# Kernel optimization log

Hardware: AMD Instinct MI355X
Metric: run time of the kernel (lower is better)

The kernel has to match this reference:

```python
import jax, jax.numpy as jnp
import numpy as np

H = W = 56
HID = 384
B = 16

def dct_mat(N):
    # Orthonormal DCT-II matrix: X = D @ x, idct via D.T
    n = jnp.arange(N, dtype=jnp.float32)
    k = jnp.arange(N, dtype=jnp.float32)[:, None]
    D = jnp.cos(jnp.pi * (2.0 * n + 1.0) * k / (2.0 * N)) * jnp.sqrt(2.0 / N)
    D = D.at[0].multiply(1.0 / jnp.sqrt(2.0))
    return D

def setup_inputs() -> dict:
    key = jax.random.key(0)
    ks = jax.random.split(key, 16)
    s = 0.02
    return {
        "x": jax.random.normal(ks[0], (B, HID, H, W), dtype=jnp.float32),
        "freq_embed": jax.random.normal(ks[1], (H, W, HID), dtype=jnp.float32),
        "dw_w": jax.random.normal(ks[2], (HID, 1, 3, 3), dtype=jnp.float32) * s,
        "dw_b": jnp.zeros((HID,), jnp.float32),
        "lin_w": jax.random.normal(ks[3], (2 * HID, HID), dtype=jnp.float32) * s,
        "lin_b": jnp.zeros((2 * HID,), jnp.float32),
        "vel_w": jax.random.normal(ks[4], (HID, HID), dtype=jnp.float32) * s,
        "vel_b": jnp.zeros((HID,), jnp.float32),
        "tok_w": jax.random.normal(ks[5], (HID, HID), dtype=jnp.float32) * s,
        "tok_b": jnp.zeros((HID,), jnp.float32),
        "ln_g": jnp.ones((HID,), jnp.float32),
        "ln_b": jnp.zeros((HID,), jnp.float32),
        "out_w": jax.random.normal(ks[6], (HID, HID), dtype=jnp.float32) * s,
        "out_b": jnp.zeros((HID,), jnp.float32),
        "c": jnp.ones((1,), jnp.float32),
        "alpha": jnp.ones((1,), jnp.float32) * 0.1,
    }

def reference(x, freq_embed, dw_w, dw_b, lin_w, lin_b, vel_w, vel_b,
              tok_w, tok_b, ln_g, ln_b, out_w, out_b, c, alpha):
    Bn, C, Hh, Ww = x.shape
    # depthwise 3x3 conv, padding=1
    x = jax.lax.conv_general_dilated(
        x, dw_w, (1, 1), 'SAME',
        dimension_numbers=('NCHW', 'OIHW', 'NCHW'),
        feature_group_count=C) + dw_b[None, :, None, None]
    xl = jnp.transpose(x, (0, 2, 3, 1))            # [B,H,W,C]
    xz = xl @ lin_w.T + lin_b                      # [B,H,W,2C]
    xg, z = jnp.split(xz, 2, axis=-1)
    DH, DW_ = dct_mat(Hh), dct_mat(Ww)
    x_ch = jnp.transpose(xg, (0, 3, 1, 2))         # [B,C,H,W]
    x_u0 = jnp.einsum('ih,jw,bchw->bcij', DH, DW_, x_ch)
    x_vel = xg @ vel_w.T + vel_b                   # [B,H,W,C]
    x_v0 = jnp.einsum('ih,jw,bchw->bcij', DH, DW_, jnp.transpose(x_vel, (0, 3, 1, 2)))
    # decay map exp(-(n^2+m^2)) on linspace(0,pi)
    wn = jnp.linspace(0.0, jnp.pi, Hh + 1)[:Hh][:, None]
    wm = jnp.linspace(0.0, jnp.pi, Ww + 1)[:Ww][None, :]
    decay = jnp.exp(-(wn ** 2 + wm ** 2))[None, None]
    x_u0 = x_u0 * decay
    x_v0 = x_v0 * decay
    # wave modulation from freq embedding (shared across batch)
    t = jax.nn.relu(freq_embed @ tok_w.T + tok_b)  # [H,W,C]
    t = jnp.transpose(t, (2, 0, 1))[None]          # [1,C,H,W]
    eps = 1e-6
    cos_t = jnp.cos(c[0] * t)
    sin_t = jnp.sin(c[0] * t) / (c[0] + eps)
    final = cos_t * x_u0 + sin_t * (x_v0 + 0.5 * alpha[0] * x_u0)
    x_final = jnp.einsum('hi,wj,bchw->bcij', DH, DW_, final)  # IDCT2D
    y = jnp.transpose(x_final, (0, 2, 3, 1))       # [B,H,W,C]
    mu = jnp.mean(y, axis=-1, keepdims=True)
    var = jnp.mean((y - mu) ** 2, axis=-1, keepdims=True)
    yn = (y - mu) / jnp.sqrt(var + 1e-5) * ln_g + ln_b
    gated = yn * jax.nn.silu(z)                    # [B,H,W,C]
    out = gated @ out_w.T + out_b
    return jnp.transpose(out, (0, 3, 1, 2))        # [B,C,H,W]
```

## Files before the change

kernel.cpp:

```cpp
#include <hip/hip_runtime.h>
#include <math.h>

#define HH 56
#define WS_W 56
#define HWS 3136
#define CD 384
#define BB 16
#define NROW (BB*HWS)
#define SLOT ((size_t)NROW*CD)

typedef __attribute__((ext_vector_type(8))) short bf16x8;
typedef __attribute__((ext_vector_type(4))) float f32x4;

__device__ inline ushort f2bf(float v) {
  uint u = __float_as_uint(v);
  uint r = (u + 0x7fffu + ((u >> 16) & 1u)) >> 16;
  return (ushort)r;
}
__device__ inline float bf2f(ushort h) { return __uint_as_float((uint)h << 16); }

__global__ void prep_d_k(float* __restrict__ D) {
  for (int idx = threadIdx.x; idx < HH*HH; idx += blockDim.x) {
    int k = idx / HH, n = idx % HH;
    double v = cos(3.14159265358979323846 * (2.0*n + 1.0) * k / (2.0*HH)) * sqrt(2.0/HH);
    if (k == 0) v *= 0.70710678118654752440;
    D[idx] = (float)v;
  }
}

__global__ __launch_bounds__(256) void split_w_k(
    const float* __restrict__ W, ushort* __restrict__ hi,
    ushort* __restrict__ lo, int nelem) {
  int i = blockIdx.x*256 + threadIdx.x;
  if (i >= nelem) return;
  float v = W[i];
  ushort h = f2bf(v);
  hi[i] = h;
  lo[i] = f2bf(v - bf2f(h));
}

__global__ __launch_bounds__(256) void conv_k(
    const float* __restrict__ x, const float* __restrict__ dww,
    const float* __restrict__ dwb, ushort* __restrict__ xc)
{
  __shared__ float xs[3][58][33];
  __shared__ float wgt[32][9];
  __shared__ float wb[32];
  int t = threadIdx.x;
  int c0 = blockIdx.x * 32, h = blockIdx.y, b = blockIdx.z;
  for (int idx = t; idx < 1344; idx += 256) {
    int wq = idx % 14, rem = idx / 14;
    int dy = rem % 3, ch = rem / 3;
    int gh = h + dy - 1;
    float4 v = {0.f, 0.f, 0.f, 0.f};
    if (gh >= 0 && gh < HH)
      v = *(const float4*)(x + (((size_t)b*CD + c0 + ch)*HH + gh)*WS_W + wq*4);
    int wp = wq*4 + 1;
    xs[dy][wp+0][ch] = v.x;
    xs[dy][wp+1][ch] = v.y;
    xs[dy][wp+2][ch] = v.z;
    xs[dy][wp+3][ch] = v.w;
  }
  if (t < 192) {
    int e = t & 1, dy = (t >> 1) % 3, ch = t / 6;
    xs[dy][e*57][ch] = 0.f;
  }
  for (int idx = t; idx < 288; idx += 256)
    wgt[idx/9][idx%9] = dww[(size_t)(c0 + idx/9)*9 + idx%9];
  if (t < 32) wb[t] = dwb[c0 + t];
  __syncthreads();
  int ch = t & 31, wq8 = t >> 5;
  #pragma unroll
  for (int wwi = 0; wwi < 7; ++wwi) {
    int w = wwi*8 + wq8;
    float acc = wb[ch];
    #pragma unroll
    for (int dy = 0; dy < 3; ++dy)
      #pragma unroll
      for (int dx = 0; dx < 3; ++dx)
        acc = fmaf(wgt[ch][dy*3+dx], xs[dy][w+dx][ch], acc);
    size_t oi = ((size_t)b*HWS + h*WS_W + w)*CD + c0 + ch;
    ushort hh = f2bf(acc);
    xc[oi] = hh;
    xc[SLOT + oi] = f2bf(acc - bf2f(hh));
  }
}

template<int EPI>
__global__ __launch_bounds__(256) void gemm_k(
    const float* __restrict__ A, const float* __restrict__ Bw,
    const float* __restrict__ bias, float* __restrict__ out0,
    float* __restrict__ out1, const float* __restrict__ cptr)
{
  __shared__ float As[16][68];
  __shared__ float Bs[16][68];
  int t = threadIdx.x;
  int col0 = blockIdx.x * 64;
  int row0 = blockIdx.y * 64;
  int lr = t >> 2, lk = (t & 3) * 4;
  const float* Ap = A + (size_t)(row0 + lr)*CD + lk;
  const float* Bp = Bw + (size_t)(col0 + lr)*CD + lk;
  float acc[4][4] = {};
  int tx = t & 15, ty = t >> 4;
  for (int k0 = 0; k0 < CD; k0 += 16) {
    float4 av = *(const float4*)(Ap + k0);
    float4 bv = *(const float4*)(Bp + k0);
    __syncthreads();
    As[lk+0][lr] = av.x; As[lk+1][lr] = av.y; As[lk+2][lr] = av.z; As[lk+3][lr] = av.w;
    Bs[lk+0][lr] = bv.x; Bs[lk+1][lr] = bv.y; Bs[lk+2][lr] = bv.z; Bs[lk+3][lr] = bv.w;
    __syncthreads();
    #pragma unroll
    for (int k = 0; k < 16; ++k) {
      float4 a4 = *(const float4*)&As[k][ty*4];
      float4 b4 = *(const float4*)&Bs[k][tx*4];
      float aa[4] = {a4.x, a4.y, a4.z, a4.w};
      float bbv[4] = {b4.x, b4.y, b4.z, b4.w};
      #pragma unroll
      for (int i = 0; i < 4; ++i)
        #pragma unroll
        for (int j = 0; j < 4; ++j)
          acc[i][j] = fmaf(aa[i], bbv[j], acc[i][j]);
    }
  }
  float cs = 0.f;
  if constexpr (EPI == 2) cs = cptr[0];
  #pragma unroll
  for (int i = 0; i < 4; ++i) {
    int r = row0 + ty*4 + i;
    #pragma unroll
    for (int j = 0; j < 4; ++j) {
      int cg = col0 + tx*4 + j;
      float v = acc[i][j];
      if constexpr (EPI == 2) {
        v += bias[cg];
        v = fmaxf(v, 0.f);
        int pi = r / 56, pj = r % 56;
        float wn = 3.14159265358979323846f/56.f * (float)pi;
        float wm = 3.14159265358979323846f/56.f * (float)pj;
        float dec = expf(-(wn*wn + wm*wm));
        out0[(size_t)r*CD + cg] = cosf(cs*v)*dec;
        out1[(size_t)r*CD + cg] = sinf(cs*v)/(cs + 1e-6f)*dec;
      }
    }
  }
}

template<int EPI>
__global__ __launch_bounds__(256, 2) void mgemm_k(
    const ushort* __restrict__ Ah_g, const ushort* __restrict__ Al_g,
    const ushort* __restrict__ Wh, const ushort* __restrict__ Wl,
    const float* __restrict__ bias,
    float* __restrict__ out0, float* __restrict__ out1,
    const ushort* __restrict__ UinH, const float* __restrict__ cosD,
    const float* __restrict__ sinD, const float* __restrict__ velb,
    const float* __restrict__ alphap)
{
  __shared__ char smem[32768];
  int t = threadIdx.x;
  int nwg = gridDim.x * gridDim.y;
  int wgid = blockIdx.y * gridDim.x + blockIdx.x;
  int cpx = nwg >> 3;
  int sw = (wgid & 7) * cpx + (wgid >> 3);
  int col0 = (sw % gridDim.x) * 128;
  int row0 = (sw / gridDim.x) * 128;

  int r = t >> 1, half = t & 1;
  int n = r & 15, rt = r >> 4, q0 = half * 2;
  const ushort* Ahp = Ah_g + (size_t)(row0 + r)*CD + half*16;
  const ushort* Alp = Al_g + (size_t)(row0 + r)*CD + half*16;
  const ushort* Bhp = Wh + (size_t)(col0 + r)*CD + half*16;
  const ushort* Blp = Wl + (size_t)(col0 + r)*CD + half*16;
  int aoff0 = rt*1024 + (q0*16 + n)*16;
  int aoff1 = rt*1024 + ((q0+1)*16 + n)*16;
  int boff0 = 16384 + aoff0, boff1 = 16384 + aoff1;
  int wid = t >> 6, lane = t & 63;
  int wr = wid >> 1, wc = wid & 1;
  f32x4 acc[4][4];
  #pragma unroll
  for (int i = 0; i < 4; ++i)
    #pragma unroll
    for (int j = 0; j < 4; ++j)
      acc[i][j] = (f32x4){0.f, 0.f, 0.f, 0.f};

  for (int k0 = 0; k0 < CD; k0 += 32) {
    uint4 fh0 = *(const uint4*)(Ahp + k0);
    uint4 fh1 = *(const uint4*)(Ahp + k0 + 8);
    uint4 fl0 = *(const uint4*)(Alp + k0);
    uint4 fl1 = *(const uint4*)(Alp + k0 + 8);
    uint4 bh0 = *(const uint4*)(Bhp + k0);
    uint4 bh1 = *(const uint4*)(Bhp + k0 + 8);
    uint4 bl0 = *(const uint4*)(Blp + k0);
    uint4 bl1 = *(const uint4*)(Blp + k0 + 8);
    __syncthreads();
    *(uint4*)(smem + aoff0)        = fh0;
    *(uint4*)(smem + aoff0 + 8192) = fl0;
    *(uint4*)(smem + aoff1)        = fh1;
    *(uint4*)(smem + aoff1 + 8192) = fl1;
    *(uint4*)(smem + boff0)        = bh0;
    *(uint4*)(smem + boff0 + 8192) = bl0;
    *(uint4*)(smem + boff1)        = bh1;
    *(uint4*)(smem + boff1 + 8192) = bl1;
    __syncthreads();
    bf16x8 Ah[4], Al[4], Bh[4], Bl[4];
    #pragma unroll
    for (int i = 0; i < 4; ++i) {
      int ao = (wr*4 + i)*1024 + lane*16;
      Ah[i] = *(const bf16x8*)(smem + ao);
      Al[i] = *(const bf16x8*)(smem + ao + 8192);
      int bo = 16384 + (wc*4 + i)*1024 + lane*16;
      Bh[i] = *(const bf16x8*)(smem + bo);
      Bl[i] = *(const bf16x8*)(smem + bo + 8192);
    }
    #pragma unroll
    for (int i = 0; i < 4; ++i)
      #pragma unroll
      for (int j = 0; j < 4; ++j) {
        acc[i][j] = __builtin_amdgcn_mfma_f32_16x16x32_bf16(Ah[i], Bh[j], acc[i][j], 0, 0, 0);
        acc[i][j] = __builtin_amdgcn_mfma_f32_16x16x32_bf16(Ah[i], Bl[j], acc[i][j], 0, 0, 0);
        acc[i][j] = __builtin_amdgcn_mfma_f32_16x16x32_bf16(Al[i], Bh[j], acc[i][j], 0, 0, 0);
      }
  }

  int nn = lane & 15, qq = lane >> 4;
  float ahalf = 0.f;
  if constexpr (EPI == 1) ahalf = 0.5f * alphap[0];
  #pragma unroll
  for (int i = 0; i < 4; ++i) {
    #pragma unroll
    for (int j = 0; j < 4; ++j) {
      #pragma unroll
      for (int reg = 0; reg < 4; ++reg) {
        int rg = row0 + wr*64 + i*16 + qq*4 + reg;
        int cg = col0 + wc*64 + j*16 + nn;
        float v = acc[i][j][reg];
        if constexpr (EPI == 0) {
          v += bias[cg];
          if (cg < CD) out0[(size_t)rg*CD + cg] = v;
          else         out1[(size_t)rg*CD + cg - CD] = v;
        } else if constexpr (EPI == 1) {
          int p = rg % HWS;
          size_t uidx = (size_t)rg*CD + cg;
          float u  = bf2f(UinH[uidx]) + bf2f(UinH[SLOT + uidx]);
          float cd = cosD[(size_t)p*CD + cg];
          float sd = sinD[(size_t)p*CD + cg];
          if (p == 0) v += 56.f * velb[cg];
          out0[uidx] = cd*u + sd*(v + ahalf*u);
        } else {
          v += bias[cg];
          int bidx = rg / HWS, hw = rg % HWS;
          out0[((size_t)bidx*CD + cg)*HWS + hw] = v;
        }
      }
    }
  }
}

__global__ __launch_bounds__(448) void dct_k(
    const float* __restrict__ in, float* __restrict__ out,
    const float* __restrict__ D, int NC, int trans, int osplit)
{
  __shared__ float Ds[56][60];
  __shared__ float Xs[56][128];
  int t = threadIdx.x;
  int c0 = blockIdx.x * 128;
  size_t bt = blockIdx.y;
  for (int idx = t; idx < 3136; idx += 448) {
    int k = idx / 56, m = idx % 56;
    Ds[k][m] = trans ? D[k*56 + m] : D[m*56 + k];
  }
  const float* inb = in + bt*56*(size_t)NC + c0;
  for (int fi = t; fi < 56*32; fi += 448) {
    int rw = fi >> 5, cg = fi & 31;
    *(float4*)&Xs[rw][cg*4] = *(const float4*)(inb + (size_t)rw*NC + cg*4);
  }
  __syncthreads();
  int tx = t % 32, ty = t / 32;
  float acc[4][4] = {};
  #pragma unroll 4
  for (int k = 0; k < 56; ++k) {
    float4 a4 = *(const float4*)&Ds[k][ty*4];
    float4 b4 = *(const float4*)&Xs[k][tx*4];
    float aa[4] = {a4.x, a4.y, a4.z, a4.w};
    float bbv[4] = {b4.x, b4.y, b4.z, b4.w};
    #pragma unroll
    for (int i = 0; i < 4; ++i)
      #pragma unroll
      for (int j = 0; j < 4; ++j)
        acc[i][j] = fmaf(aa[i], bbv[j], acc[i][j]);
  }
  if (!osplit) {
    float* ob = out + bt*56*(size_t)NC + c0;
    #pragma unroll
    for (int i = 0; i < 4; ++i) {
      int m = ty*4 + i;
      float4 o; o.x = acc[i][0]; o.y = acc[i][1]; o.z = acc[i][2]; o.w = acc[i][3];
      *(float4*)(ob + (size_t)m*NC + tx*4) = o;
    }
  } else {
    ushort* obh = (ushort*)out;
    size_t base = bt*56*(size_t)NC + c0;
    #pragma unroll
    for (int i = 0; i < 4; ++i) {
      int m = ty*4 + i;
      size_t e = base + (size_t)m*NC + tx*4;
      ushort hs[4], ls[4];
      #pragma unroll
      for (int j = 0; j < 4; ++j) {
        float v = acc[i][j];
        hs[j] = f2bf(v);
        ls[j] = f2bf(v - bf2f(hs[j]));
      }
      uint2 hv, lv;
      hv.x = hs[0] | ((uint)hs[1] << 16); hv.y = hs[2] | ((uint)hs[3] << 16);
      lv.x = ls[0] | ((uint)ls[1] << 16); lv.y = ls[2] | ((uint)ls[3] << 16);
      *(uint2*)(obh + e) = hv;
      *(uint2*)(obh + SLOT + e) = lv;
    }
  }
}

__global__ __launch_bounds__(256) void ln_gate_k(
    const float* __restrict__ Y, const float* __restrict__ Z,
    const float* __restrict__ g, const float* __restrict__ be,
    ushort* __restrict__ out)
{
  int lane = threadIdx.x & 63, wv = threadIdx.x >> 6;
  size_t r = (size_t)blockIdx.x*4 + wv;
  const float* y = Y + r*CD;
  float v[6];
  float s = 0.f;
  #pragma unroll
  for (int q = 0; q < 6; ++q) { v[q] = y[lane + 64*q]; s += v[q]; }
  #pragma unroll
  for (int off = 32; off > 0; off >>= 1) s += __shfl_xor(s, off, 64);
  float mu = s * (1.f/384.f);
  float s2 = 0.f;
  #pragma unroll
  for (int q = 0; q < 6; ++q) { float d = v[q]-mu; s2 += d*d; }
  #pragma unroll
  for (int off = 32; off > 0; off >>= 1) s2 += __shfl_xor(s2, off, 64);
  float rs = 1.f / sqrtf(s2*(1.f/384.f) + 1e-5f);
  #pragma unroll
  for (int q = 0; q < 6; ++q) {
    int c = lane + 64*q;
    float yn = (v[q]-mu)*rs*g[c] + be[c];
    float zv = Z[r*CD + c];
    float sz = zv / (1.f + expf(-zv));
    float gv = yn*sz;
    ushort hh = f2bf(gv);
    out[r*CD + c] = hh;
    out[SLOT + r*CD + c] = f2bf(gv - bf2f(hh));
  }
}

extern "C" void kernel_launch(void* const* d_in, const int* in_sizes, int n_in,
                              void* d_out, int out_size, void* d_ws, size_t ws_size,
                              hipStream_t stream) {
  const float* x     = (const float*)d_in[0];
  const float* fe    = (const float*)d_in[1];
  const float* dw_w  = (const float*)d_in[2];
  const float* dw_b  = (const float*)d_in[3];
  const float* lin_w = (const float*)d_in[4];
  const float* lin_b = (const float*)d_in[5];
  const float* vel_w = (const float*)d_in[6];
  const float* vel_b = (const float*)d_in[7];
  const float* tok_w = (const float*)d_in[8];
  const float* tok_b = (const float*)d_in[9];
  const float* ln_g  = (const float*)d_in[10];
  const float* ln_b  = (const float*)d_in[11];
  const float* out_w = (const float*)d_in[12];
  const float* out_b = (const float*)d_in[13];
  const float* cp    = (const float*)d_in[14];
  const float* ap    = (const float*)d_in[15];

  float* ws    = (float*)d_ws;
  float* slotA = ws;
  float* slotB = ws + SLOT;
  float* slotC = ws + 2*SLOT;
  float* Dm    = ws + 3*SLOT;
  float* cosD  = Dm + 3136;
  float* sinD  = cosD + (size_t)HWS*CD;
  ushort* whi  = (ushort*)(sinD + (size_t)HWS*CD);
  ushort* wlo  = whi + 589824;

  ushort* xcH = (ushort*)slotA;
  ushort* UH  = (ushort*)slotB;
  ushort* GH  = (ushort*)slotB;

  prep_d_k<<<1, 256, 0, stream>>>(Dm);
  split_w_k<<<1152, 256, 0, stream>>>(lin_w, whi,          wlo,          294912);
  split_w_k<<< 576, 256, 0, stream>>>(vel_w, whi + 294912, wlo + 294912, 147456);
  split_w_k<<< 576, 256, 0, stream>>>(out_w, whi + 442368, wlo + 442368, 147456);

  conv_k<<<dim3(12, 56, 16), 256, 0, stream>>>(x, dw_w, dw_b, xcH);
  gemm_k<2><<<dim3(6, 49), 256, 0, stream>>>(fe, tok_w, tok_b, cosD, sinD, cp);
  mgemm_k<0><<<dim3(6, 392), 256, 0, stream>>>(xcH, xcH + SLOT, whi, wlo, lin_b,
      slotB, slotC, nullptr, nullptr, nullptr, nullptr, nullptr);
  dct_k<<<dim3(168, 16), 448, 0, stream>>>(slotB, slotA, Dm, 21504, 0, 0);
  dct_k<<<dim3(3, 896), 448, 0, stream>>>(slotA, slotB, Dm, 384, 0, 1);
  mgemm_k<1><<<dim3(3, 392), 256, 0, stream>>>(UH, UH + SLOT, whi + 294912, wlo + 294912,
      nullptr, slotA, nullptr, UH, cosD, sinD, vel_b, ap);
  dct_k<<<dim3(168, 16), 448, 0, stream>>>(slotA, slotB, Dm, 21504, 1, 0);
  dct_k<<<dim3(3, 896), 448, 0, stream>>>(slotB, slotA, Dm, 384, 1, 0);
  ln_gate_k<<<12544, 256, 0, stream>>>(slotA, slotC, ln_g, ln_b, GH);
  mgemm_k<3><<<dim3(3, 392), 256, 0, stream>>>(GH, GH + SLOT, whi + 442368, wlo + 442368,
      out_b, (float*)d_out, nullptr, nullptr, nullptr, nullptr, nullptr, nullptr);
}
```

Baseline: 744.5 us.

## Fuse separable DCT passes into single 2D DCT kernel with blocked channel layout

Replaces the two separable 1D DCT launches (forward and inverse) with one dct2d kernel per direction. Each block loads a full 56x56 plane for four channels into shared memory and applies both passes there, which removes the intermediate global round trip. The forward output is written in a channel-blocked (groups of 8) bf16 hi/lo layout, so the velocity GEMM gains a new A-operand addressing mode and an updated epilogue index. The cost is heavy shared-memory use with only 56 of 64 lanes active, and strided A loads in the GEMM.

```diff
diff --git a/kernel.cpp b/kernel.cpp
--- a/kernel.cpp
+++ b/kernel.cpp
@@ -145,7 +145,7 @@
   }
 }
 
-template<int EPI>
+template<int EPI, int ALAY>
 __global__ __launch_bounds__(256, 2) void mgemm_k(
     const ushort* __restrict__ Ah_g, const ushort* __restrict__ Al_g,
     const ushort* __restrict__ Wh, const ushort* __restrict__ Wl,
@@ -166,8 +166,16 @@
 
   int r = t >> 1, half = t & 1;
   int n = r & 15, rt = r >> 4, q0 = half * 2;
-  const ushort* Ahp = Ah_g + (size_t)(row0 + r)*CD + half*16;
-  const ushort* Alp = Al_g + (size_t)(row0 + r)*CD + half*16;
+  const ushort* Ahp; const ushort* Alp;
+  if constexpr (ALAY == 0) {
+    Ahp = Ah_g + (size_t)(row0 + r)*CD + half*16;
+    Alp = Al_g + (size_t)(row0 + r)*CD + half*16;
+  } else {
+    int rg = row0 + r; int bb = rg / HWS, p = rg % HWS;
+    size_t base = ((size_t)(bb*48 + half*2)*HWS + p)*8;
+    Ahp = Ah_g + base;
+    Alp = Al_g + base;
+  }
   const ushort* Bhp = Wh + (size_t)(col0 + r)*CD + half*16;
   const ushort* Blp = Wl + (size_t)(col0 + r)*CD + half*16;
   int aoff0 = rt*1024 + (q0*16 + n)*16;
@@ -183,10 +191,19 @@
       acc[i][j] = (f32x4){0.f, 0.f, 0.f, 0.f};
 
   for (int k0 = 0; k0 < CD; k0 += 32) {
-    uint4 fh0 = *(const uint4*)(Ahp + k0);
-    uint4 fh1 = *(const uint4*)(Ahp + k0 + 8);
-    uint4 fl0 = *(const uint4*)(Alp + k0);
-    uint4 fl1 = *(const uint4*)(Alp + k0 + 8);
+    uint4 fh0, fh1, fl0, fl1;
+    if constexpr (ALAY == 0) {
+      fh0 = *(const uint4*)(Ahp + k0);
+      fh1 = *(const uint4*)(Ahp + k0 + 8);
+      fl0 = *(const uint4*)(Alp + k0);
+      fl1 = *(const uint4*)(Alp + k0 + 8);
+    } else {
+      size_t o = (size_t)k0 * HWS;
+      fh0 = *(const uint4*)(Ahp + o);
+      fh1 = *(const uint4*)(Ahp + o + HWS*8);
+      fl0 = *(const uint4*)(Alp + o);
+      fl1 = *(const uint4*)(Alp + o + HWS*8);
+    }
     uint4 bh0 = *(const uint4*)(Bhp + k0);
     uint4 bh1 = *(const uint4*)(Bhp + k0 + 8);
     uint4 bl0 = *(const uint4*)(Blp + k0);
@@ -238,8 +255,8 @@
           if (cg < CD) out0[(size_t)rg*CD + cg] = v;
           else         out1[(size_t)rg*CD + cg - CD] = v;
         } else if constexpr (EPI == 1) {
-          int p = rg % HWS;
-          size_t uidx = (size_t)rg*CD + cg;
+          int p = rg % HWS, bidx = rg / HWS;
+          size_t uidx = ((size_t)(bidx*48 + (cg >> 3))*HWS + p)*8 + (cg & 7);
           float u  = bf2f(UinH[uidx]) + bf2f(UinH[SLOT + uidx]);
           float cd = cosD[(size_t)p*CD + cg];
           float sd = sinD[(size_t)p*CD + cg];
@@ -255,66 +272,136 @@
   }
 }
 
-__global__ __launch_bounds__(448) void dct_k(
+template<int INV>
+__global__ __launch_bounds__(256, 2) void dct2d_k(
     const float* __restrict__ in, float* __restrict__ out,
-    const float* __restrict__ D, int NC, int trans, int osplit)
+    const float* __restrict__ Dm)
 {
-  __shared__ float Ds[56][60];
-  __shared__ float Xs[56][128];
+  __shared__ float Xs[4*3364];
+  __shared__ float M1[3360];
+  __shared__ float M2[3360];
   int t = threadIdx.x;
-  int c0 = blockIdx.x * 128;
-  size_t bt = blockIdx.y;
-  for (int idx = t; idx < 3136; idx += 448) {
-    int k = idx / 56, m = idx % 56;
-    Ds[k][m] = trans ? D[k*56 + m] : D[m*56 + k];
-  }
-  const float* inb = in + bt*56*(size_t)NC + c0;
-  for (int fi = t; fi < 56*32; fi += 448) {
-    int rw = fi >> 5, cg = fi & 31;
-    *(float4*)&Xs[rw][cg*4] = *(const float4*)(inb + (size_t)rw*NC + cg*4);
+  int xb = blockIdx.x;
+  int cg4 = (xb & 7)*12 + (xb >> 3);
+  int b = blockIdx.y;
+  int cb8 = cg4 >> 1, sub4 = (cg4 & 1)*4, c0 = cg4*4;
+
+  for (int idx = t; idx < 3136; idx += 256) {
+    int r_ = idx/56, q_ = idx%56;
+    float dv = Dm[r_*56 + q_];
+    if (INV) { M1[r_*60 + q_] = dv; M2[q_*60 + r_] = dv; }
+    else     { M1[q_*60 + r_] = dv; M2[r_*60 + q_] = dv; }
+  }
+  if (INV) {
+    const float* Fb = in + ((size_t)(b*48 + cb8)*HWS)*8 + sub4;
+    for (int p = t; p < HWS; p += 256) {
+      float4 v = *(const float4*)(Fb + (size_t)p*8);
+      int h = p/56, w = p%56;
+      Xs[0*3364 + h*60 + w] = v.x;
+      Xs[1*3364 + h*60 + w] = v.y;
+      Xs[2*3364 + h*60 + w] = v.z;
+      Xs[3*3364 + h*60 + w] = v.w;
+    }
+  } else {
+    const float* inb = in + (size_t)b*HWS*CD + c0;
+    for (int p = t; p < HWS; p += 256) {
+      float4 v = *(const float4*)(inb + (size_t)p*CD);
+      int h = p/56, w = p%56;
+      Xs[0*3364 + h*60 + w] = v.x;
+      Xs[1*3364 + h*60 + w] = v.y;
+      Xs[2*3364 + h*60 + w] = v.z;
+      Xs[3*3364 + h*60 + w] = v.w;
+    }
   }
   __syncthreads();
-  int tx = t % 32, ty = t / 32;
-  float acc[4][4] = {};
-  #pragma unroll 4
-  for (int k = 0; k < 56; ++k) {
-    float4 a4 = *(const float4*)&Ds[k][ty*4];
-    float4 b4 = *(const float4*)&Xs[k][tx*4];
-    float aa[4] = {a4.x, a4.y, a4.z, a4.w};
-    float bbv[4] = {b4.x, b4.y, b4.z, b4.w};
-    #pragma unroll
-    for (int i = 0; i < 4; ++i)
-      #pragma unroll
-      for (int j = 0; j < 4; ++j)
-        acc[i][j] = fmaf(aa[i], bbv[j], acc[i][j]);
-  }
-  if (!osplit) {
-    float* ob = out + bt*56*(size_t)NC + c0;
-    #pragma unroll
-    for (int i = 0; i < 4; ++i) {
-      int m = ty*4 + i;
-      float4 o; o.x = acc[i][0]; o.y = acc[i][1]; o.z = acc[i][2]; o.w = acc[i][3];
-      *(float4*)(ob + (size_t)m*NC + tx*4) = o;
+
+  int ch = t >> 6, l = t & 63;
+  int jg = l % 14, hg = l / 14;
+  float a2[14][4];
+  if (l < 56) {
+    float* Xc = &Xs[ch*3364];
+    float acc[14][4] = {};
+    for (int w = 0; w < 56; ++w) {
+      float4 m = *(const float4*)&M1[w*60 + jg*4];
+      #pragma unroll
+      for (int ri = 0; ri < 14; ++ri) {
+        float xv = Xc[(hg*14 + ri)*60 + w];
+        acc[ri][0] = fmaf(xv, m.x, acc[ri][0]);
+        acc[ri][1] = fmaf(xv, m.y, acc[ri][1]);
+        acc[ri][2] = fmaf(xv, m.z, acc[ri][2]);
+        acc[ri][3] = fmaf(xv, m.w, acc[ri][3]);
+      }
+    }
+    #pragma unroll
+    for (int ri = 0; ri < 14; ++ri) {
+      float4 o = {acc[ri][0], acc[ri][1], acc[ri][2], acc[ri][3]};
+      *(float4*)&Xc[(hg*14 + ri)*60 + jg*4] = o;
+    }
+    #pragma unroll
+    for (int ri = 0; ri < 14; ++ri) { a2[ri][0]=0.f; a2[ri][1]=0.f; a2[ri][2]=0.f; a2[ri][3]=0.f; }
+    for (int h = 0; h < 56; ++h) {
+      float4 tv = *(const float4*)&Xc[h*60 + jg*4];
+      #pragma unroll
+      for (int ri = 0; ri < 14; ++ri) {
+        float dv = M2[(hg*14 + ri)*60 + h];
+        a2[ri][0] = fmaf(dv, tv.x, a2[ri][0]);
+        a2[ri][1] = fmaf(dv, tv.y, a2[ri][1]);
+        a2[ri][2] = fmaf(dv, tv.z, a2[ri][2]);
+        a2[ri][3] = fmaf(dv, tv.w, a2[ri][3]);
+      }
+    }
+  }
+  __syncthreads();
+  if (l < 56) {
+    if (INV) {
+      float* Yl = Xs;
+      #pragma unroll
+      for (int ri = 0; ri < 14; ++ri) {
+        int p = (hg*14 + ri)*56 + jg*4;
+        float4 o = {a2[ri][0], a2[ri][1], a2[ri][2], a2[ri][3]};
+        *(float4*)&Yl[ch*3140 + p] = o;
+      }
+    } else {
+      ushort* Ul = (ushort*)Xs;
+      #pragma unroll
+      for (int ri = 0; ri < 14; ++ri) {
+        int p = (hg*14 + ri)*56 + jg*4;
+        ushort hs[4], ls[4];
+        #pragma unroll
+        for (int dj = 0; dj < 4; ++dj) {
+          float v = a2[ri][dj];
+          hs[dj] = f2bf(v);
+          ls[dj] = f2bf(v - bf2f(hs[dj]));
+        }
+        uint2 hv, lv;
+        hv.x = hs[0] | ((uint)hs[1] << 16); hv.y = hs[2] | ((uint)hs[3] << 16);
+        lv.x = ls[0] | ((uint)ls[1] << 16); lv.y = ls[2] | ((uint)ls[3] << 16);
+        *(uint2*)&Ul[ch*3136 + p] = hv;
+        *(uint2*)&Ul[12544 + ch*3136 + p] = lv;
+      }
+    }
+  }
+  __syncthreads();
+  if (INV) {
+    const float* Yl = Xs;
+    float* ob = out + (size_t)b*HWS*CD + c0;
+    for (int p = t; p < HWS; p += 256) {
+      float4 o = {Yl[0*3140 + p], Yl[1*3140 + p], Yl[2*3140 + p], Yl[3*3140 + p]};
+      *(float4*)(ob + (size_t)p*CD) = o;
     }
   } else {
-    ushort* obh = (ushort*)out;
-    size_t base = bt*56*(size_t)NC + c0;
-    #pragma unroll
-    for (int i = 0; i < 4; ++i) {
-      int m = ty*4 + i;
-      size_t e = base + (size_t)m*NC + tx*4;
-      ushort hs[4], ls[4];
-      #pragma unroll
-      for (int j = 0; j < 4; ++j) {
-        float v = acc[i][j];
-        hs[j] = f2bf(v);
-        ls[j] = f2bf(v - bf2f(hs[j]));
-      }
-      uint2 hv, lv;
-      hv.x = hs[0] | ((uint)hs[1] << 16); hv.y = hs[2] | ((uint)hs[3] << 16);
-      lv.x = ls[0] | ((uint)ls[1] << 16); lv.y = ls[2] | ((uint)ls[3] << 16);
-      *(uint2*)(obh + e) = hv;
-      *(uint2*)(obh + SLOT + e) = lv;
+    const ushort* Ul = (const ushort*)Xs;
+    ushort* og = (ushort*)out;
+    size_t base = ((size_t)(b*48 + cb8)*HWS)*8 + sub4;
+    for (int idx = t; idx < 2*HWS; idx += 256) {
+      int pl = idx >= HWS;
+      int p = pl ? idx - HWS : idx;
+      ushort u0 = Ul[pl*12544 + 0*3136 + p];
+      ushort u1 = Ul[pl*12544 + 1*3136 + p];
+      ushort u2 = Ul[pl*12544 + 2*3136 + p];
+      ushort u3 = Ul[pl*12544 + 3*3136 + p];
+      uint2 v; v.x = u0 | ((uint)u1 << 16); v.y = u2 | ((uint)u3 << 16);
+      *(uint2*)(og + (size_t)pl*SLOT + base + (size_t)p*8) = v;
     }
   }
 }
@@ -384,7 +471,7 @@
   ushort* wlo  = whi + 589824;
 
   ushort* xcH = (ushort*)slotA;
-  ushort* UH  = (ushort*)slotB;
+  ushort* UH  = (ushort*)slotA;
   ushort* GH  = (ushort*)slotB;
 
   prep_d_k<<<1, 256, 0, stream>>>(Dm);
@@ -394,15 +481,13 @@
 
   conv_k<<<dim3(12, 56, 16), 256, 0, stream>>>(x, dw_w, dw_b, xcH);
   gemm_k<2><<<dim3(6, 49), 256, 0, stream>>>(fe, tok_w, tok_b, cosD, sinD, cp);
-  mgemm_k<0><<<dim3(6, 392), 256, 0, stream>>>(xcH, xcH + SLOT, whi, wlo, lin_b,
+  mgemm_k<0,0><<<dim3(6, 392), 256, 0, stream>>>(xcH, xcH + SLOT, whi, wlo, lin_b,
       slotB, slotC, nullptr, nullptr, nullptr, nullptr, nullptr);
-  dct_k<<<dim3(168, 16), 448, 0, stream>>>(slotB, slotA, Dm, 21504, 0, 0);
-  dct_k<<<dim3(3, 896), 448, 0, stream>>>(slotA, slotB, Dm, 384, 0, 1);
-  mgemm_k<1><<<dim3(3, 392), 256, 0, stream>>>(UH, UH + SLOT, whi + 294912, wlo + 294912,
-      nullptr, slotA, nullptr, UH, cosD, sinD, vel_b, ap);
-  dct_k<<<dim3(168, 16), 448, 0, stream>>>(slotA, slotB, Dm, 21504, 1, 0);
-  dct_k<<<dim3(3, 896), 448, 0, stream>>>(slotB, slotA, Dm, 384, 1, 0);
+  dct2d_k<0><<<dim3(96, 16), 256, 0, stream>>>(slotB, slotA, Dm);
+  mgemm_k<1,1><<<dim3(3, 392), 256, 0, stream>>>(UH, UH + SLOT, whi + 294912, wlo + 294912,
+      nullptr, slotB, nullptr, UH, cosD, sinD, vel_b, ap);
+  dct2d_k<1><<<dim3(96, 16), 256, 0, stream>>>(slotB, slotA, Dm);
   ln_gate_k<<<12544, 256, 0, stream>>>(slotA, slotC, ln_g, ln_b, GH);
-  mgemm_k<3><<<dim3(3, 392), 256, 0, stream>>>(GH, GH + SLOT, whi + 442368, wlo + 442368,
+  mgemm_k<3,0><<<dim3(3, 392), 256, 0, stream>>>(GH, GH + SLOT, whi + 442368, wlo + 442368,
       out_b, (float*)d_out, nullptr, nullptr, nullptr, nullptr, nullptr, nullptr);
 }
```

Measured after the change: 749.9 us. Within noise of the previous version (+0.7%).

## Run DCT transforms on bf16 MFMA with hi/lo split-precision

Applied to the files above, without the earlier changes.

Replaces the four scalar-FMA DCT matrix-multiply kernels with an MFMA-based kernel. Each fp32 operand is split into bf16 hi and lo parts and the product is summed over four MFMA passes to keep near-fp32 accuracy. The DCT matrix is pre-packed into a padded 64x64 swizzled layout and loaded into LDS with global_load_lds. Blocks are remapped with a swizzle for cache locality. This shifts the DCT work off the vector ALUs onto matrix cores, at the cost of extra conversion work, padding waste from 56 to 64, and uncoalesced scalar output stores.

```diff
diff --git a/kernel.cpp b/kernel.cpp
--- a/kernel.cpp
+++ b/kernel.cpp
@@ -19,12 +19,34 @@
 }
 __device__ inline float bf2f(ushort h) { return __uint_as_float((uint)h << 16); }
 
+__device__ inline void gl16(const void* g, void* l) {
+  __builtin_amdgcn_global_load_lds(
+      (const __attribute__((address_space(1))) void*)g,
+      (__attribute__((address_space(3))) void*)l,
+      16, 0, 0);
+}
+
 __global__ void prep_d_k(float* __restrict__ D) {
   for (int idx = threadIdx.x; idx < HH*HH; idx += blockDim.x) {
     int k = idx / HH, n = idx % HH;
     double v = cos(3.14159265358979323846 * (2.0*n + 1.0) * k / (2.0*HH)) * sqrt(2.0/HH);
     if (k == 0) v *= 0.70710678118654752440;
     D[idx] = (float)v;
+  }
+}
+
+__global__ void prep_pack_k(const float* __restrict__ Dm, ushort* __restrict__ Dpk) {
+  for (int idx = threadIdx.x; idx < 2*4096; idx += 256) {
+    int o = idx >> 12, e = idx & 4095;
+    int mg = e >> 10, rem = e & 1023;
+    int j = rem & 7, km = rem >> 3;
+    int koct = km >> 4, m16 = km & 15;
+    int m = mg*16 + m16, k = koct*8 + j;
+    float v = 0.f;
+    if (m < 56 && k < 56) v = o ? Dm[k*56 + m] : Dm[m*56 + k];
+    ushort h = f2bf(v);
+    Dpk[o*8192 + e] = h;
+    Dpk[o*8192 + 4096 + e] = f2bf(v - bf2f(h));
   }
 }
 
@@ -255,66 +277,105 @@
   }
 }
 
-__global__ __launch_bounds__(448) void dct_k(
-    const float* __restrict__ in, float* __restrict__ out,
-    const float* __restrict__ D, int NC, int trans, int osplit)
+template<int OSPLIT>
+__global__ __launch_bounds__(256, 3) void dmm_k(
+    const float* __restrict__ in, float* __restrict__ outf,
+    const ushort* __restrict__ Dpk, int NBT, int RS, size_t BSTR)
 {
-  __shared__ float Ds[56][60];
-  __shared__ float Xs[56][128];
+  __shared__ char smem[49152];
   int t = threadIdx.x;
-  int c0 = blockIdx.x * 128;
-  size_t bt = blockIdx.y;
-  for (int idx = t; idx < 3136; idx += 448) {
-    int k = idx / 56, m = idx % 56;
-    Ds[k][m] = trans ? D[k*56 + m] : D[m*56 + k];
-  }
-  const float* inb = in + bt*56*(size_t)NC + c0;
-  for (int fi = t; fi < 56*32; fi += 448) {
-    int rw = fi >> 5, cg = fi & 31;
-    *(float4*)&Xs[rw][cg*4] = *(const float4*)(inb + (size_t)rw*NC + cg*4);
-  }
-  __syncthreads();
-  int tx = t % 32, ty = t / 32;
-  float acc[4][4] = {};
-  #pragma unroll 4
-  for (int k = 0; k < 56; ++k) {
-    float4 a4 = *(const float4*)&Ds[k][ty*4];
-    float4 b4 = *(const float4*)&Xs[k][tx*4];
-    float aa[4] = {a4.x, a4.y, a4.z, a4.w};
-    float bbv[4] = {b4.x, b4.y, b4.z, b4.w};
+  int flat = blockIdx.x;
+  int sw = (flat & 7) * 336 + (flat >> 3);
+  int batch = sw / NBT, nt0 = sw - batch*NBT;
+  int n0 = nt0 * 128;
+  const float* inb = in + (size_t)batch*BSTR;
+  int wid = t >> 6, lane = t & 63;
+
+  {
+    const char* src = (const char*)Dpk;
     #pragma unroll
     for (int i = 0; i < 4; ++i)
-      #pragma unroll
-      for (int j = 0; j < 4; ++j)
-        acc[i][j] = fmaf(aa[i], bbv[j], acc[i][j]);
-  }
-  if (!osplit) {
-    float* ob = out + bt*56*(size_t)NC + c0;
-    #pragma unroll
-    for (int i = 0; i < 4; ++i) {
-      int m = ty*4 + i;
-      float4 o; o.x = acc[i][0]; o.y = acc[i][1]; o.z = acc[i][2]; o.w = acc[i][3];
-      *(float4*)(ob + (size_t)m*NC + tx*4) = o;
-    }
-  } else {
-    ushort* obh = (ushort*)out;
-    size_t base = bt*56*(size_t)NC + c0;
-    #pragma unroll
-    for (int i = 0; i < 4; ++i) {
-      int m = ty*4 + i;
-      size_t e = base + (size_t)m*NC + tx*4;
-      ushort hs[4], ls[4];
-      #pragma unroll
-      for (int j = 0; j < 4; ++j) {
-        float v = acc[i][j];
+      gl16(src + wid*4096 + i*1024 + lane*16,
+           smem + 32768 + wid*4096 + i*1024);
+  }
+
+  {
+    int koct = t >> 5, c4 = (t & 31) * 4;
+    float4 fr[8];
+    if (koct < 7) {
+      #pragma unroll
+      for (int j = 0; j < 8; ++j)
+        fr[j] = *(const float4*)(inb + (size_t)(koct*8 + j)*RS + n0 + c4);
+    } else {
+      #pragma unroll
+      for (int j = 0; j < 8; ++j) fr[j] = (float4){0.f,0.f,0.f,0.f};
+    }
+    #pragma unroll
+    for (int c = 0; c < 4; ++c) {
+      ushort hs[8], ls[8];
+      #pragma unroll
+      for (int j = 0; j < 8; ++j) {
+        float v = ((const float*)&fr[j])[c];
         hs[j] = f2bf(v);
         ls[j] = f2bf(v - bf2f(hs[j]));
       }
-      uint2 hv, lv;
-      hv.x = hs[0] | ((uint)hs[1] << 16); hv.y = hs[2] | ((uint)hs[3] << 16);
-      lv.x = ls[0] | ((uint)ls[1] << 16); lv.y = ls[2] | ((uint)ls[3] << 16);
-      *(uint2*)(obh + e) = hv;
-      *(uint2*)(obh + SLOT + e) = lv;
+      uint4 hv, lv;
+      hv.x = hs[0]|((uint)hs[1]<<16); hv.y = hs[2]|((uint)hs[3]<<16);
+      hv.z = hs[4]|((uint)hs[5]<<16); hv.w = hs[6]|((uint)hs[7]<<16);
+      lv.x = ls[0]|((uint)ls[1]<<16); lv.y = ls[2]|((uint)ls[3]<<16);
+      lv.z = ls[4]|((uint)ls[5]<<16); lv.w = ls[6]|((uint)ls[7]<<16);
+      int nn = c4 + c;
+      int off = (nn >> 4)*2048 + (koct*16 + ((nn & 15) ^ koct))*16;
+      *(uint4*)(smem + off)         = hv;
+      *(uint4*)(smem + 16384 + off) = lv;
+    }
+  }
+  __syncthreads();
+
+  int mg = wid;
+  bf16x8 Ah[2], Al[2];
+  #pragma unroll
+  for (int ks = 0; ks < 2; ++ks) {
+    int ao = 32768 + mg*2048 + ((ks*4 + (lane>>4))*16 + (lane&15))*16;
+    Ah[ks] = *(const bf16x8*)(smem + ao);
+    Al[ks] = *(const bf16x8*)(smem + ao + 8192);
+  }
+  f32x4 acc[8];
+  #pragma unroll
+  for (int nt = 0; nt < 8; ++nt) acc[nt] = (f32x4){0.f,0.f,0.f,0.f};
+  #pragma unroll
+  for (int nt = 0; nt < 8; ++nt) {
+    #pragma unroll
+    for (int ks = 0; ks < 2; ++ks) {
+      int koctr = ks*4 + (lane>>4);
+      int bo = nt*2048 + (koctr*16 + ((lane & 15) ^ koctr))*16;
+      bf16x8 Bh = *(const bf16x8*)(smem + bo);
+      bf16x8 Bl = *(const bf16x8*)(smem + bo + 16384);
+      acc[nt] = __builtin_amdgcn_mfma_f32_16x16x32_bf16(Ah[ks], Bh, acc[nt], 0, 0, 0);
+      acc[nt] = __builtin_amdgcn_mfma_f32_16x16x32_bf16(Ah[ks], Bl, acc[nt], 0, 0, 0);
+      acc[nt] = __builtin_amdgcn_mfma_f32_16x16x32_bf16(Al[ks], Bh, acc[nt], 0, 0, 0);
+      acc[nt] = __builtin_amdgcn_mfma_f32_16x16x32_bf16(Al[ks], Bl, acc[nt], 0, 0, 0);
+    }
+  }
+
+  int q = lane >> 4, n16 = lane & 15;
+  #pragma unroll
+  for (int nt = 0; nt < 8; ++nt) {
+    #pragma unroll
+    for (int reg = 0; reg < 4; ++reg) {
+      int m = mg*16 + q*4 + reg;
+      if (m < 56) {
+        size_t addr = (size_t)batch*BSTR + (size_t)m*RS + n0 + nt*16 + n16;
+        float v = acc[nt][reg];
+        if constexpr (OSPLIT == 0) {
+          outf[addr] = v;
+        } else {
+          ushort* oh = (ushort*)outf;
+          ushort hh = f2bf(v);
+          oh[addr] = hh;
+          oh[SLOT + addr] = f2bf(v - bf2f(hh));
+        }
+      }
     }
   }
 }
@@ -382,12 +443,14 @@
   float* sinD  = cosD + (size_t)HWS*CD;
   ushort* whi  = (ushort*)(sinD + (size_t)HWS*CD);
   ushort* wlo  = whi + 589824;
+  ushort* Dpk  = wlo + 589824;
 
   ushort* xcH = (ushort*)slotA;
   ushort* UH  = (ushort*)slotB;
   ushort* GH  = (ushort*)slotB;
 
   prep_d_k<<<1, 256, 0, stream>>>(Dm);
+  prep_pack_k<<<1, 256, 0, stream>>>(Dm, Dpk);
   split_w_k<<<1152, 256, 0, stream>>>(lin_w, whi,          wlo,          294912);
   split_w_k<<< 576, 256, 0, stream>>>(vel_w, whi + 294912, wlo + 294912, 147456);
   split_w_k<<< 576, 256, 0, stream>>>(out_w, whi + 442368, wlo + 442368, 147456);
@@ -396,12 +459,12 @@
   gemm_k<2><<<dim3(6, 49), 256, 0, stream>>>(fe, tok_w, tok_b, cosD, sinD, cp);
   mgemm_k<0><<<dim3(6, 392), 256, 0, stream>>>(xcH, xcH + SLOT, whi, wlo, lin_b,
       slotB, slotC, nullptr, nullptr, nullptr, nullptr, nullptr);
-  dct_k<<<dim3(168, 16), 448, 0, stream>>>(slotB, slotA, Dm, 21504, 0, 0);
-  dct_k<<<dim3(3, 896), 448, 0, stream>>>(slotA, slotB, Dm, 384, 0, 1);
+  dmm_k<0><<<2688, 256, 0, stream>>>(slotB, slotA, Dpk,        168, 21504, (size_t)1204224);
+  dmm_k<1><<<2688, 256, 0, stream>>>(slotA, slotB, Dpk,          3,   384, (size_t)21504);
   mgemm_k<1><<<dim3(3, 392), 256, 0, stream>>>(UH, UH + SLOT, whi + 294912, wlo + 294912,
       nullptr, slotA, nullptr, UH, cosD, sinD, vel_b, ap);
-  dct_k<<<dim3(168, 16), 448, 0, stream>>>(slotA, slotB, Dm, 21504, 1, 0);
-  dct_k<<<dim3(3, 896), 448, 0, stream>>>(slotB, slotA, Dm, 384, 1, 0);
+  dmm_k<0><<<2688, 256, 0, stream>>>(slotA, slotB, Dpk + 8192, 168, 21504, (size_t)1204224);
+  dmm_k<0><<<2688, 256, 0, stream>>>(slotB, slotA, Dpk + 8192,   3,   384, (size_t)21504);
   ln_gate_k<<<12544, 256, 0, stream>>>(slotA, slotC, ln_g, ln_b, GH);
   mgemm_k<3><<<dim3(3, 392), 256, 0, stream>>>(GH, GH + SLOT, whi + 442368, wlo + 442368,
       out_b, (float*)d_out, nullptr, nullptr, nullptr, nullptr, nullptr, nullptr);
```

Result: faster. 678.8 us (-8.8%).
